# Kernel optimization log

Hardware: AMD Instinct MI355X
Metric: run time of the kernel (lower is better)

## Reference

```python
import jax, jax.numpy as jnp
import numpy as np
from jax import lax

NUM_STEPS = 20
BATCH, DIM, HID = 4096, 512, 2048


def setup_inputs() -> dict:
    key = jax.random.key(0)
    k_z, k_w1, k_w2 = jax.random.split(key, 3)
    z0 = jax.random.normal(k_z, (BATCH, DIM), dtype=jnp.float32)
    # fan-in scaled weights so the ODE dynamics stay well-conditioned
    W1 = jax.random.normal(k_w1, (DIM + 1, HID), dtype=jnp.float32) * (1.0 / np.sqrt(DIM + 1))
    b1 = jnp.zeros((HID,), dtype=jnp.float32)
    W2 = jax.random.normal(k_w2, (HID, DIM), dtype=jnp.float32) * (0.1 / np.sqrt(HID))
    b2 = jnp.zeros((DIM,), dtype=jnp.float32)
    t0 = jnp.zeros((), dtype=jnp.float32)
    t1 = jnp.ones((), dtype=jnp.float32)
    return {"z0": z0, "W1": W1, "b1": b1, "W2": W2, "b2": b2, "t0": t0, "t1": t1}


def reference(z0, W1, b1, W2, b2, t0, t1):
    h = (t1 - t0) / NUM_STEPS

    def func(z, t):
        # time broadcast to [batch, 1], concatenated to the state (Neural-ODE MLP dynamics)
        tb = jnp.full((z.shape[0], 1), t, dtype=z.dtype)
        hidden = jnp.tanh(jnp.concatenate([z, tb], axis=-1) @ W1 + b1)
        return hidden @ W2 + b2

    def step(z, i):
        t = t0 + i * h
        k1 = func(z, t)
        k2 = func(z + 0.5 * h * k1, t + 0.5 * h)
        k3 = func(z + 0.5 * h * k2, t + 0.5 * h)
        k4 = func(z + h * k3, t + h)
        z_next = z + (h / 6.0) * (k1 + 2.0 * k2 + 2.0 * k3 + k4)
        return z_next, None

    z, _ = lax.scan(step, z0, jnp.arange(NUM_STEPS, dtype=z0.dtype))
    return z
```

## Files before the change

kernel.cpp:

```cpp
#include <hip/hip_runtime.h>
#include <hip/hip_bf16.h>

#define BATCH 4096
#define DIM   512
#define HID   2048
#define NSTEPS 20

typedef __attribute__((ext_vector_type(8))) short short8;
typedef __attribute__((ext_vector_type(4))) short short4v;
typedef __attribute__((ext_vector_type(4))) float floatx4;

__device__ __forceinline__ short f2bf(float x) {
    union { float f; unsigned u; } v; v.f = x;
    unsigned r = v.u + 0x7fffu + ((v.u >> 16) & 1u);
    return (short)(r >> 16);
}

__device__ __forceinline__ float fast_tanh(float x) {
    float e = __builtin_amdgcn_exp2f(x * 2.8853900817779268f);
    float r = __builtin_amdgcn_rcpf(1.0f + e);
    return 1.0f - 2.0f * r;
}

__global__ void transpose_cvt(const float* __restrict__ src, short* __restrict__ dst,
                              int K, int N) {
    __shared__ float tile[32][33];
    int k0 = blockIdx.x * 32, n0 = blockIdx.y * 32;
    int tx = threadIdx.x, ty = threadIdx.y;
    #pragma unroll
    for (int r = ty; r < 32; r += 8)
        tile[r][tx] = src[(size_t)(k0 + r) * N + n0 + tx];
    __syncthreads();
    #pragma unroll
    for (int r = ty; r < 32; r += 8)
        dst[(size_t)(n0 + r) * K + k0 + tx] = f2bf(tile[tx][r]);
}

__global__ void extract_row(const float* __restrict__ W1, float* __restrict__ w1last) {
    int i = blockIdx.x * 256 + threadIdx.x;
    w1last[i] = W1[(size_t)DIM * HID + i];
}

__global__ void init_abuf(const float* __restrict__ z0, short* __restrict__ abuf) {
    size_t i = (size_t)(blockIdx.x * 256 + threadIdx.x) * 4;
    float4 zv = *(const float4*)(z0 + i);
    short4v o;
    o[0] = f2bf(zv.x); o[1] = f2bf(zv.y); o[2] = f2bf(zv.z); o[3] = f2bf(zv.w);
    *(short4v*)(abuf + i) = o;
}

__global__ __launch_bounds__(256, 2)
void gemm1_tanh(const short* __restrict__ A, const short* __restrict__ Bt,
                const float* __restrict__ b1, const float* __restrict__ w1last,
                const float* __restrict__ t0p, const float* __restrict__ t1p,
                float c_t, float step_i,
                short* __restrict__ hidden) {
    __shared__ short Alds[128 * 64];
    __shared__ short Blds[128 * 64];
    const int tid = threadIdx.x;
    const int lane = tid & 63;
    const int wave = tid >> 6;
    const int wm = wave >> 1, wn = wave & 1;
    const int bm0 = blockIdx.x * 128;
    const int bn0 = blockIdx.y * 128;

    const float t0 = t0p[0], t1 = t1p[0];
    const float h = (t1 - t0) / (float)NSTEPS;
    const float teval = t0 + (step_i + c_t) * h;

    floatx4 acc[4][4];
    #pragma unroll
    for (int i = 0; i < 4; i++)
        #pragma unroll
        for (int j = 0; j < 4; j++) acc[i][j] = (floatx4)0.f;

    const int fr = lane & 15;
    const int fkc = lane >> 4;
    const int rx = fr & 7;

    for (int kk = 0; kk < DIM; kk += 64) {
        #pragma unroll
        for (int p = 0; p < 4; p++) {
            int c = tid + p * 256;
            int row = c >> 3;
            int g = (c & 7) ^ (row & 7);
            const short* gpA = A + (size_t)(bm0 + row) * DIM + kk + g * 8;
            __builtin_amdgcn_global_load_lds(
                (const __attribute__((address_space(1))) void*)gpA,
                (__attribute__((address_space(3))) void*)&Alds[c * 8], 16, 0, 0);
            const short* gpB = Bt + (size_t)(bn0 + row) * DIM + kk + g * 8;
            __builtin_amdgcn_global_load_lds(
                (const __attribute__((address_space(1))) void*)gpB,
                (__attribute__((address_space(3))) void*)&Blds[c * 8], 16, 0, 0);
        }
        __syncthreads();
        #pragma unroll
        for (int s = 0; s < 2; s++) {
            const int slot = ((s * 4 + fkc) ^ rx) * 8;
            short8 af[4], bfr[4];
            #pragma unroll
            for (int mt = 0; mt < 4; mt++)
                af[mt] = *(const short8*)&Alds[(wm * 64 + mt * 16 + fr) * 64 + slot];
            #pragma unroll
            for (int nt = 0; nt < 4; nt++)
                bfr[nt] = *(const short8*)&Blds[(wn * 64 + nt * 16 + fr) * 64 + slot];
            #pragma unroll
            for (int mt = 0; mt < 4; mt++)
                #pragma unroll
                for (int nt = 0; nt < 4; nt++)
                    acc[mt][nt] = __builtin_amdgcn_mfma_f32_16x16x32_bf16(af[mt], bfr[nt], acc[mt][nt], 0, 0, 0);
        }
        __syncthreads();
    }
    #pragma unroll
    for (int nt = 0; nt < 4; nt++) {
        int col = bn0 + wn * 64 + nt * 16 + fr;
        float c1 = b1[col] + teval * w1last[col];
        #pragma unroll
        for (int mt = 0; mt < 4; mt++) {
            int row0 = bm0 + wm * 64 + mt * 16 + fkc * 4;
            #pragma unroll
            for (int r = 0; r < 4; r++) {
                float v = acc[mt][nt][r] + c1;
                hidden[(size_t)(row0 + r) * HID + col] = f2bf(fast_tanh(v));
            }
        }
    }
}

__global__ __launch_bounds__(256, 2)
void gemm2_fused(const short* __restrict__ hidden,
                 const short* __restrict__ Bt,
                 const float* __restrict__ b2,
                 float* __restrict__ z,
                 float* __restrict__ kacc, short* __restrict__ abuf,
                 const float* __restrict__ t0p, const float* __restrict__ t1p,
                 int mode, float wk, float alpha_c) {
    __shared__ short lds[4 * 8192];
    const int tid = threadIdx.x;
    const int lane = tid & 63;
    const int wave = tid >> 6;
    const int bm0 = blockIdx.x * 64;
    const int bn0 = blockIdx.y * 64;
    const int kbase = wave * 512;

    short* slabA = &lds[wave * 8192];
    short* slabB = slabA + 4096;

    const int fr = lane & 15;
    const int fkc = lane >> 4;
    const int rx = fr & 7;
    const int l3 = lane >> 3;
    const int gch = (lane & 7) ^ l3;

    floatx4 acc[4][4];
    #pragma unroll
    for (int i = 0; i < 4; i++)
        #pragma unroll
        for (int j = 0; j < 4; j++) acc[i][j] = (floatx4)0.f;

    for (int kk = 0; kk < 512; kk += 64) {
        const int k0 = kbase + kk;
        __builtin_amdgcn_s_waitcnt(0xC07F);
        #pragma unroll
        for (int j = 0; j < 8; j++) {
            int row = j * 8 + l3;
            const short* gpA = hidden + (size_t)(bm0 + row) * HID + k0 + gch * 8;
            __builtin_amdgcn_global_load_lds(
                (const __attribute__((address_space(1))) void*)gpA,
                (__attribute__((address_space(3))) void*)&slabA[j * 512 + lane * 8], 16, 0, 0);
            const short* gpB = Bt + (size_t)(bn0 + row) * HID + k0 + gch * 8;
            __builtin_amdgcn_global_load_lds(
                (const __attribute__((address_space(1))) void*)gpB,
                (__attribute__((address_space(3))) void*)&slabB[j * 512 + lane * 8], 16, 0, 0);
        }
        __builtin_amdgcn_sched_barrier(0);
        __builtin_amdgcn_s_waitcnt(0x0F70);
        __builtin_amdgcn_sched_barrier(0);
        #pragma unroll
        for (int s = 0; s < 2; s++) {
            const int slot = ((s * 4 + fkc) ^ rx) * 8;
            short8 af[4], bfr[4];
            #pragma unroll
            for (int mt = 0; mt < 4; mt++)
                af[mt] = *(const short8*)&slabA[(mt * 16 + fr) * 64 + slot];
            #pragma unroll
            for (int nt = 0; nt < 4; nt++)
                bfr[nt] = *(const short8*)&slabB[(nt * 16 + fr) * 64 + slot];
            #pragma unroll
            for (int mt = 0; mt < 4; mt++)
                #pragma unroll
                for (int nt = 0; nt < 4; nt++)
                    acc[mt][nt] = __builtin_amdgcn_mfma_f32_16x16x32_bf16(af[mt], bfr[nt], acc[mt][nt], 0, 0, 0);
        }
        __builtin_amdgcn_sched_barrier(0);
    }

    float* fslab = (float*)slabA;
    #pragma unroll
    for (int mt = 0; mt < 4; mt++)
        #pragma unroll
        for (int nt = 0; nt < 4; nt++)
            #pragma unroll
            for (int r = 0; r < 4; r++) {
                int row = mt * 16 + fkc * 4 + r;
                int col = nt * 16 + fr;
                fslab[row * 64 + col] = acc[mt][nt][r];
            }
    __syncthreads();

    const int rrow = tid >> 2;
    const int cb = (tid & 3) * 16;
    float4 v[4];
    #pragma unroll
    for (int ch = 0; ch < 4; ch++) v[ch] = make_float4(0.f, 0.f, 0.f, 0.f);
    #pragma unroll
    for (int w = 0; w < 4; w++) {
        const float* fs = (const float*)&lds[w * 8192];
        #pragma unroll
        for (int ch = 0; ch < 4; ch++) {
            float4 p = *(const float4*)&fs[rrow * 64 + cb + ch * 4];
            v[ch].x += p.x; v[ch].y += p.y; v[ch].z += p.z; v[ch].w += p.w;
        }
    }

    const float h = (t1p[0] - t0p[0]) / (float)NSTEPS;
    const float ah = alpha_c * h;
    const float h6 = h / 6.0f;
    const size_t base = (size_t)(bm0 + rrow) * DIM + bn0 + cb;
    #pragma unroll
    for (int ch = 0; ch < 4; ch++) {
        float4 bb = *(const float4*)&b2[bn0 + cb + ch * 4];
        float kv[4] = { v[ch].x + bb.x, v[ch].y + bb.y, v[ch].z + bb.z, v[ch].w + bb.w };
        size_t idx = base + ch * 4;
        float4 zv = *(const float4*)&z[idx];
        float zn[4];
        if (mode == 0) {
            *(float4*)&kacc[idx] = make_float4(kv[0], kv[1], kv[2], kv[3]);
            zn[0] = zv.x + ah * kv[0]; zn[1] = zv.y + ah * kv[1];
            zn[2] = zv.z + ah * kv[2]; zn[3] = zv.w + ah * kv[3];
        } else if (mode == 1) {
            float4 ka = *(const float4*)&kacc[idx];
            *(float4*)&kacc[idx] = make_float4(ka.x + wk * kv[0], ka.y + wk * kv[1],
                                               ka.z + wk * kv[2], ka.w + wk * kv[3]);
            zn[0] = zv.x + ah * kv[0]; zn[1] = zv.y + ah * kv[1];
            zn[2] = zv.z + ah * kv[2]; zn[3] = zv.w + ah * kv[3];
        } else {
            float4 ka = *(const float4*)&kacc[idx];
            zn[0] = zv.x + h6 * (ka.x + kv[0]); zn[1] = zv.y + h6 * (ka.y + kv[1]);
            zn[2] = zv.z + h6 * (ka.z + kv[2]); zn[3] = zv.w + h6 * (ka.w + kv[3]);
            *(float4*)&z[idx] = make_float4(zn[0], zn[1], zn[2], zn[3]);
        }
        short4v o;
        o[0] = f2bf(zn[0]); o[1] = f2bf(zn[1]); o[2] = f2bf(zn[2]); o[3] = f2bf(zn[3]);
        *(short4v*)&abuf[idx] = o;
    }
}

extern "C" void kernel_launch(void* const* d_in, const int* in_sizes, int n_in,
                              void* d_out, int out_size, void* d_ws, size_t ws_size,
                              hipStream_t stream) {
    const float* z0  = (const float*)d_in[0];
    const float* W1  = (const float*)d_in[1];
    const float* b1  = (const float*)d_in[2];
    const float* W2  = (const float*)d_in[3];
    const float* b2  = (const float*)d_in[4];
    const float* t0p = (const float*)d_in[5];
    const float* t1p = (const float*)d_in[6];
    float* z = (float*)d_out;

    char* ws = (char*)d_ws;
    short* W1t    = (short*)(ws);
    short* W2t    = (short*)(ws + (2u << 20));
    float* w1last = (float*)(ws + (4u << 20));
    short* abuf   = (short*)(ws + (4u << 20) + (1u << 16));
    short* hidden = (short*)(ws + (8u << 20) + (1u << 16));
    float* kacc   = (float*)(ws + (24u << 20) + (1u << 16));

    hipMemcpyAsync(z, z0, (size_t)BATCH * DIM * sizeof(float),
                   hipMemcpyDeviceToDevice, stream);
    transpose_cvt<<<dim3(DIM / 32, HID / 32), dim3(32, 8), 0, stream>>>(W1, W1t, DIM, HID);
    transpose_cvt<<<dim3(HID / 32, DIM / 32), dim3(32, 8), 0, stream>>>(W2, W2t, HID, DIM);
    extract_row<<<HID / 256, 256, 0, stream>>>(W1, w1last);
    init_abuf<<<BATCH * DIM / 4 / 256, 256, 0, stream>>>(z0, abuf);

    const dim3 g1(BATCH / 128, HID / 128), g2(BATCH / 64, DIM / 64), b(256);
    for (int i = 0; i < NSTEPS; i++) {
        float fi = (float)i;
        gemm1_tanh<<<g1, b, 0, stream>>>(abuf, W1t, b1, w1last, t0p, t1p, 0.0f, fi, hidden);
        gemm2_fused<<<g2, b, 0, stream>>>(hidden, W2t, b2, z, kacc, abuf, t0p, t1p, 0, 1.0f, 0.5f);
        gemm1_tanh<<<g1, b, 0, stream>>>(abuf, W1t, b1, w1last, t0p, t1p, 0.5f, fi, hidden);
        gemm2_fused<<<g2, b, 0, stream>>>(hidden, W2t, b2, z, kacc, abuf, t0p, t1p, 1, 2.0f, 0.5f);
        gemm1_tanh<<<g1, b, 0, stream>>>(abuf, W1t, b1, w1last, t0p, t1p, 0.5f, fi, hidden);
        gemm2_fused<<<g2, b, 0, stream>>>(hidden, W2t, b2, z, kacc, abuf, t0p, t1p, 1, 2.0f, 1.0f);
        gemm1_tanh<<<g1, b, 0, stream>>>(abuf, W1t, b1, w1last, t0p, t1p, 1.0f, fi, hidden);
        gemm2_fused<<<g2, b, 0, stream>>>(hidden, W2t, b2, z, kacc, abuf, t0p, t1p, 2, 1.0f, 0.0f);
    }
}
```

Baseline: 3.100 ms.

## Double-buffer LDS tiles in both GEMMs and vectorize tanh epilogue stores

```diff
diff --git a/kernel.cpp b/kernel.cpp
--- a/kernel.cpp
+++ b/kernel.cpp
@@ -9,6 +9,10 @@
 typedef __attribute__((ext_vector_type(8))) short short8;
 typedef __attribute__((ext_vector_type(4))) short short4v;
 typedef __attribute__((ext_vector_type(4))) float floatx4;
+
+#define GLL(dst, src) __builtin_amdgcn_global_load_lds( \
+    (const __attribute__((address_space(1))) void*)(src), \
+    (__attribute__((address_space(3))) void*)(dst), 16, 0, 0)
 
 __device__ __forceinline__ short f2bf(float x) {
     union { float f; unsigned u; } v; v.f = x;
@@ -55,8 +59,8 @@
                 const float* __restrict__ t0p, const float* __restrict__ t1p,
                 float c_t, float step_i,
                 short* __restrict__ hidden) {
-    __shared__ short Alds[128 * 64];
-    __shared__ short Blds[128 * 64];
+    __shared__ short Alds[2][128 * 64];
+    __shared__ short Blds[2][128 * 64];
     const int tid = threadIdx.x;
     const int lane = tid & 63;
     const int wave = tid >> 6;
@@ -78,52 +82,56 @@
     const int fkc = lane >> 4;
     const int rx = fr & 7;
 
-    for (int kk = 0; kk < DIM; kk += 64) {
+    auto stage = [&](int it, int bufi) {
+        const int kk = it * 64;
         #pragma unroll
         for (int p = 0; p < 4; p++) {
             int c = tid + p * 256;
             int row = c >> 3;
             int g = (c & 7) ^ (row & 7);
-            const short* gpA = A + (size_t)(bm0 + row) * DIM + kk + g * 8;
-            __builtin_amdgcn_global_load_lds(
-                (const __attribute__((address_space(1))) void*)gpA,
-                (__attribute__((address_space(3))) void*)&Alds[c * 8], 16, 0, 0);
-            const short* gpB = Bt + (size_t)(bn0 + row) * DIM + kk + g * 8;
-            __builtin_amdgcn_global_load_lds(
-                (const __attribute__((address_space(1))) void*)gpB,
-                (__attribute__((address_space(3))) void*)&Blds[c * 8], 16, 0, 0);
-        }
+            GLL(&Alds[bufi][c * 8], A  + (size_t)(bm0 + row) * DIM + kk + g * 8);
+            GLL(&Blds[bufi][c * 8], Bt + (size_t)(bn0 + row) * DIM + kk + g * 8);
+        }
+    };
+
+    stage(0, 0);
+    for (int it = 0; it < 8; ++it) {
         __syncthreads();
+        if (it < 7) stage(it + 1, (it + 1) & 1);
+        const short* Ab = Alds[it & 1];
+        const short* Bb = Blds[it & 1];
         #pragma unroll
         for (int s = 0; s < 2; s++) {
             const int slot = ((s * 4 + fkc) ^ rx) * 8;
             short8 af[4], bfr[4];
             #pragma unroll
             for (int mt = 0; mt < 4; mt++)
-                af[mt] = *(const short8*)&Alds[(wm * 64 + mt * 16 + fr) * 64 + slot];
+                af[mt] = *(const short8*)&Ab[(wm * 64 + mt * 16 + fr) * 64 + slot];
             #pragma unroll
             for (int nt = 0; nt < 4; nt++)
-                bfr[nt] = *(const short8*)&Blds[(wn * 64 + nt * 16 + fr) * 64 + slot];
+                bfr[nt] = *(const short8*)&Bb[(wn * 64 + nt * 16 + fr) * 64 + slot];
             #pragma unroll
             for (int mt = 0; mt < 4; mt++)
                 #pragma unroll
                 for (int nt = 0; nt < 4; nt++)
-                    acc[mt][nt] = __builtin_amdgcn_mfma_f32_16x16x32_bf16(af[mt], bfr[nt], acc[mt][nt], 0, 0, 0);
-        }
-        __syncthreads();
-    }
-    #pragma unroll
-    for (int nt = 0; nt < 4; nt++) {
-        int col = bn0 + wn * 64 + nt * 16 + fr;
-        float c1 = b1[col] + teval * w1last[col];
-        #pragma unroll
-        for (int mt = 0; mt < 4; mt++) {
-            int row0 = bm0 + wm * 64 + mt * 16 + fkc * 4;
-            #pragma unroll
-            for (int r = 0; r < 4; r++) {
-                float v = acc[mt][nt][r] + c1;
-                hidden[(size_t)(row0 + r) * HID + col] = f2bf(fast_tanh(v));
-            }
+                    acc[mt][nt] = __builtin_amdgcn_mfma_f32_16x16x32_bf16(bfr[nt], af[mt], acc[mt][nt], 0, 0, 0);
+        }
+    }
+    #pragma unroll
+    for (int mt = 0; mt < 4; mt++) {
+        int m = bm0 + wm * 64 + mt * 16 + fr;
+        short* hrow = hidden + (size_t)m * HID;
+        #pragma unroll
+        for (int nt = 0; nt < 4; nt++) {
+            int n0 = bn0 + wn * 64 + nt * 16 + fkc * 4;
+            float4 bb = *(const float4*)&b1[n0];
+            float4 wl = *(const float4*)&w1last[n0];
+            short4v o;
+            o[0] = f2bf(fast_tanh(acc[mt][nt][0] + bb.x + teval * wl.x));
+            o[1] = f2bf(fast_tanh(acc[mt][nt][1] + bb.y + teval * wl.y));
+            o[2] = f2bf(fast_tanh(acc[mt][nt][2] + bb.z + teval * wl.z));
+            o[3] = f2bf(fast_tanh(acc[mt][nt][3] + bb.w + teval * wl.w));
+            *(short4v*)&hrow[n0] = o;
         }
     }
 }
@@ -136,22 +144,19 @@
                  float* __restrict__ kacc, short* __restrict__ abuf,
                  const float* __restrict__ t0p, const float* __restrict__ t1p,
                  int mode, float wk, float alpha_c) {
-    __shared__ short lds[4 * 8192];
+    __shared__ short lds[32768];
     const int tid = threadIdx.x;
     const int lane = tid & 63;
     const int wave = tid >> 6;
     const int bm0 = blockIdx.x * 64;
     const int bn0 = blockIdx.y * 64;
     const int kbase = wave * 512;
-
-    short* slabA = &lds[wave * 8192];
-    short* slabB = slabA + 4096;
+    short* wbase = &lds[wave * 8192];
 
     const int fr = lane & 15;
     const int fkc = lane >> 4;
-    const int rx = fr & 7;
-    const int l3 = lane >> 3;
-    const int gch = (lane & 7) ^ l3;
+    const int l2r = lane >> 2;
+    const int lch = lane & 3;
 
     floatx4 acc[4][4];
     #pragma unroll
@@ -159,44 +164,40 @@
         #pragma unroll
         for (int j = 0; j < 4; j++) acc[i][j] = (floatx4)0.f;
 
-    for (int kk = 0; kk < 512; kk += 64) {
-        const int k0 = kbase + kk;
-        __builtin_amdgcn_s_waitcnt(0xC07F);
-        #pragma unroll
-        for (int j = 0; j < 8; j++) {
-            int row = j * 8 + l3;
-            const short* gpA = hidden + (size_t)(bm0 + row) * HID + k0 + gch * 8;
-            __builtin_amdgcn_global_load_lds(
-                (const __attribute__((address_space(1))) void*)gpA,
-                (__attribute__((address_space(3))) void*)&slabA[j * 512 + lane * 8], 16, 0, 0);
-            const short* gpB = Bt + (size_t)(bn0 + row) * HID + k0 + gch * 8;
-            __builtin_amdgcn_global_load_lds(
-                (const __attribute__((address_space(1))) void*)gpB,
-                (__attribute__((address_space(3))) void*)&slabB[j * 512 + lane * 8], 16, 0, 0);
-        }
-        __builtin_amdgcn_sched_barrier(0);
-        __builtin_amdgcn_s_waitcnt(0x0F70);
-        __builtin_amdgcn_sched_barrier(0);
-        #pragma unroll
-        for (int s = 0; s < 2; s++) {
-            const int slot = ((s * 4 + fkc) ^ rx) * 8;
-            short8 af[4], bfr[4];
-            #pragma unroll
-            for (int mt = 0; mt < 4; mt++)
-                af[mt] = *(const short8*)&slabA[(mt * 16 + fr) * 64 + slot];
+    auto issue = [&](int it, int bufi) {
+        short* sA = wbase + bufi * 4096;
+        short* sB = sA + 2048;
+        const int k0 = kbase + it * 32;
+        #pragma unroll
+        for (int j = 0; j < 4; j++) {
+            int row = j * 16 + l2r;
+            GLL(&sA[j * 512 + lane * 8], hidden + (size_t)(bm0 + row) * HID + k0 + lch * 8);
+            GLL(&sB[j * 512 + lane * 8], Bt     + (size_t)(bn0 + row) * HID + k0 + lch * 8);
+        }
+    };
+
+    issue(0, 0);
+    for (int it = 0; it < 16; ++it) {
+        __syncthreads();
+        if (it < 15) issue(it + 1, (it + 1) & 1);
+        const short* sA = wbase + (it & 1) * 4096;
+        const short* sB = sA + 2048;
+        short8 af[4], bfr[4];
+        #pragma unroll
+        for (int mt = 0; mt < 4; mt++)
+            af[mt] = *(const short8*)&sA[(mt * 16 + fr) * 32 + fkc * 8];
+        #pragma unroll
+        for (int nt = 0; nt < 4; nt++)
+            bfr[nt] = *(const short8*)&sB[(nt * 16 + fr) * 32 + fkc * 8];
+        #pragma unroll
+        for (int mt = 0; mt < 4; mt++)
             #pragma unroll
             for (int nt = 0; nt < 4; nt++)
-                bfr[nt] = *(const short8*)&slabB[(nt * 16 + fr) * 64 + slot];
-            #pragma unroll
-            for (int mt = 0; mt < 4; mt++)
-                #pragma unroll
-                for (int nt = 0; nt < 4; nt++)
-                    acc[mt][nt] = __builtin_amdgcn_mfma_f32_16x16x32_bf16(af[mt], bfr[nt], acc[mt][nt], 0, 0, 0);
-        }
-        __builtin_amdgcn_sched_barrier(0);
-    }
-
-    float* fslab = (float*)slabA;
+                acc[mt][nt] = __builtin_amdgcn_mfma_f32_16x16x32_bf16(af[mt], bfr[nt], acc[mt][nt], 0, 0, 0);
+    }
+
+    __syncthreads();
+    float* fslab = (float*)wbase;
     #pragma unroll
     for (int mt = 0; mt < 4; mt++)
         #pragma unroll
```

Result: slower. 3.605 ms (+16.3%).

## Shrink gemm1 N-tile to 64, swap MFMA operands for vectorized epilogue stores

Applied to the files above, without the earlier changes.

```diff
diff --git a/kernel.cpp b/kernel.cpp
--- a/kernel.cpp
+++ b/kernel.cpp
@@ -9,6 +9,10 @@
 typedef __attribute__((ext_vector_type(8))) short short8;
 typedef __attribute__((ext_vector_type(4))) short short4v;
 typedef __attribute__((ext_vector_type(4))) float floatx4;
+
+#define GLL(dst, src) __builtin_amdgcn_global_load_lds( \
+    (const __attribute__((address_space(1))) void*)(src), \
+    (__attribute__((address_space(3))) void*)(dst), 16, 0, 0)
 
 __device__ __forceinline__ short f2bf(float x) {
     union { float f; unsigned u; } v; v.f = x;
@@ -49,30 +53,31 @@
     *(short4v*)(abuf + i) = o;
 }
 
-__global__ __launch_bounds__(256, 2)
+__global__ __launch_bounds__(256, 4)
 void gemm1_tanh(const short* __restrict__ A, const short* __restrict__ Bt,
                 const float* __restrict__ b1, const float* __restrict__ w1last,
                 const float* __restrict__ t0p, const float* __restrict__ t1p,
                 float c_t, float step_i,
                 short* __restrict__ hidden) {
     __shared__ short Alds[128 * 64];
-    __shared__ short Blds[128 * 64];
+    __shared__ short Blds[64 * 64];
     const int tid = threadIdx.x;
     const int lane = tid & 63;
     const int wave = tid >> 6;
     const int wm = wave >> 1, wn = wave & 1;
     const int bm0 = blockIdx.x * 128;
-    const int bn0 = blockIdx.y * 128;
+    const int bn0 = blockIdx.y * 64;
 
     const float t0 = t0p[0], t1 = t1p[0];
     const float h = (t1 - t0) / (float)NSTEPS;
     const float teval = t0 + (step_i + c_t) * h;
 
-    floatx4 acc[4][4];
-    #pragma unroll
-    for (int i = 0; i < 4; i++)
-        #pragma unroll
-        for (int j = 0; j < 4; j++) acc[i][j] = (floatx4)0.f;
+    floatx4 acc[4][2];
+    #pragma unroll
+    for (int i = 0; i < 4; i++) {
+        acc[i][0] = (floatx4)0.f;
+        acc[i][1] = (floatx4)0.f;
+    }
 
     const int fr = lane & 15;
     const int fkc = lane >> 4;
@@ -84,46 +89,48 @@
             int c = tid + p * 256;
             int row = c >> 3;
             int g = (c & 7) ^ (row & 7);
-            const short* gpA = A + (size_t)(bm0 + row) * DIM + kk + g * 8;
-            __builtin_amdgcn_global_load_lds(
-                (const __attribute__((address_space(1))) void*)gpA,
-                (__attribute__((address_space(3))) void*)&Alds[c * 8], 16, 0, 0);
-            const short* gpB = Bt + (size_t)(bn0 + row) * DIM + kk + g * 8;
-            __builtin_amdgcn_global_load_lds(
-                (const __attribute__((address_space(1))) void*)gpB,
-                (__attribute__((address_space(3))) void*)&Blds[c * 8], 16, 0, 0);
+            GLL(&Alds[c * 8], A + (size_t)(bm0 + row) * DIM + kk + g * 8);
+        }
+        #pragma unroll
+        for (int p = 0; p < 2; p++) {
+            int c = tid + p * 256;
+            int row = c >> 3;
+            int g = (c & 7) ^ (row & 7);
+            GLL(&Blds[c * 8], Bt + (size_t)(bn0 + row) * DIM + kk + g * 8);
         }
         __syncthreads();
         #pragma unroll
         for (int s = 0; s < 2; s++) {
             const int slot = ((s * 4 + fkc) ^ rx) * 8;
-            short8 af[4], bfr[4];
-            #pragma unroll
-            for (int mt = 0; mt < 4; mt++)
-                af[mt] = *(const short8*)&Alds[(wm * 64 + mt * 16 + fr) * 64 + slot];
-            #pragma unroll
-            for (int nt = 0; nt < 4; nt++)
-                bfr[nt] = *(const short8*)&Blds[(wn * 64 + nt * 16 + fr) * 64 + slot];
-            #pragma unroll
-            for (int mt = 0; mt < 4; mt++)
+            short8 bfr[2];
+            #pragma unroll
+            for (int nt = 0; nt < 2; nt++)
+                bfr[nt] = *(const short8*)&Blds[(wn * 32 + nt * 16 + fr) * 64 + slot];
+            #pragma unroll
+            for (int mt = 0; mt < 4; mt++) {
+                short8 af = *(const short8*)&Alds[(wm * 64 + mt * 16 + fr) * 64 + slot];
                 #pragma unroll
-                for (int nt = 0; nt < 4; nt++)
-                    acc[mt][nt] = __builtin_amdgcn_mfma_f32_16x16x32_bf16(af[mt], bfr[nt], acc[mt][nt], 0, 0, 0);
+                for (int nt = 0; nt < 2; nt++)
+                    acc[mt][nt] = __builtin_amdgcn_mfma_f32_16x16x32_bf16(bfr[nt], af, acc[mt][nt], 0, 0, 0);
+            }
         }
         __syncthreads();
     }
     #pragma unroll
-    for (int nt = 0; nt < 4; nt++) {
-        int col = bn0 + wn * 64 + nt * 16 + fr;
-        float c1 = b1[col] + teval * w1last[col];
-        #pragma unroll
-        for (int mt = 0; mt < 4; mt++) {
-            int row0 = bm0 + wm * 64 + mt * 16 + fkc * 4;
-            #pragma unroll
-            for (int r = 0; r < 4; r++) {
-                float v = acc[mt][nt][r] + c1;
-                hidden[(size_t)(row0 + r) * HID + col] = f2bf(fast_tanh(v));
-            }
+    for (int mt = 0; mt < 4; mt++) {
+        int m = bm0 + wm * 64 + mt * 16 + fr;
+        short* hrow = hidden + (size_t)m * HID;
+        #pragma unroll
+        for (int nt = 0; nt < 2; nt++) {
+            int n0 = bn0 + wn * 32 + nt * 16 + fkc * 4;
+            float4 bb = *(const float4*)&b1[n0];
+            float4 wl = *(const float4*)&w1last[n0];
+            short4v o;
+            o[0] = f2bf(fast_tanh(acc[mt][nt][0] + bb.x + teval * wl.x));
+            o[1] = f2bf(fast_tanh(acc[mt][nt][1] + bb.y + teval * wl.y));
+            o[2] = f2bf(fast_tanh(acc[mt][nt][2] + bb.z + teval * wl.z));
+            o[3] = f2bf(fast_tanh(acc[mt][nt][3] + bb.w + teval * wl.w));
+            *(short4v*)&hrow[n0] = o;
         }
     }
 }
@@ -165,14 +172,8 @@
         #pragma unroll
         for (int j = 0; j < 8; j++) {
             int row = j * 8 + l3;
-            const short* gpA = hidden + (size_t)(bm0 + row) * HID + k0 + gch * 8;
-            __builtin_amdgcn_global_load_lds(
-                (const __attribute__((address_space(1))) void*)gpA,
-                (__attribute__((address_space(3))) void*)&slabA[j * 512 + lane * 8], 16, 0, 0);
-            const short* gpB = Bt + (size_t)(bn0 + row) * HID + k0 + gch * 8;
-            __builtin_amdgcn_global_load_lds(
-                (const __attribute__((address_space(1))) void*)gpB,
-                (__attribute__((address_space(3))) void*)&slabB[j * 512 + lane * 8], 16, 0, 0);
+            GLL(&slabA[j * 512 + lane * 8], hidden + (size_t)(bm0 + row) * HID + k0 + gch * 8);
+            GLL(&slabB[j * 512 + lane * 8], Bt     + (size_t)(bn0 + row) * HID + k0 + gch * 8);
         }
         __builtin_amdgcn_sched_barrier(0);
         __builtin_amdgcn_s_waitcnt(0x0F70);
@@ -284,7 +285,7 @@
     extract_row<<<HID / 256, 256, 0, stream>>>(W1, w1last);
     init_abuf<<<BATCH * DIM / 4 / 256, 256, 0, stream>>>(z0, abuf);
 
-    const dim3 g1(BATCH / 128, HID / 128), g2(BATCH / 64, DIM / 64), b(256);
+    const dim3 g1(BATCH / 128, HID / 64), g2(BATCH / 64, DIM / 64), b(256);
     for (int i = 0; i < NSTEPS; i++) {
         float fi = (float)i;
         gemm1_tanh<<<g1, b, 0, stream>>>(abuf, W1t, b1, w1last, t0p, t1p, 0.0f, fi, hidden);
```

Result: no change. 3.145 ms (+1.5%).
